# Kernel tuning notes

Hardware: AMD Instinct MI355X
Metric: run time of the kernel (lower is better)

Reference implementation:

```python
import jax, jax.numpy as jnp
import numpy as np
from collections import defaultdict

H = 24; W = 24          # patch grid
B0 = 64                 # original batch (len(batch_id))
B = 128                 # total batch incl. augmented copies
C_IN = 256; HID = 128; HEADS_S = 2; OUT = 256; K = 9; NCLS = 8


def _build_space_edges():
    # knn_graph on the normalized meshgrid coords; identical for every image -> offset copies.
    P = H * W
    coords = np.stack(np.meshgrid(np.arange(H), np.arange(W), indexing='ij'), -1).reshape(-1, 2).astype(np.float32)
    cn = coords / coords.max()
    d = ((cn[:, None, :] - cn[None, :, :]) ** 2).sum(-1)
    np.fill_diagonal(d, np.inf)              # loop=False
    nbr = np.argsort(d, axis=1)[:, :K]       # [P, K] neighbor (source) ids
    off = (np.arange(B0) * P)[:, None, None]
    src = (nbr[None] + off).reshape(-1)
    dst = (np.broadcast_to(np.arange(P)[:, None], (P, K))[None] + off).reshape(-1)
    return np.stack([src, dst]).astype(np.int64)


def _build_view_edges(bid_all):
    groups = defaultdict(list)
    for i, c in enumerate(bid_all.tolist()):
        groups[c].append(i)
    ei = []
    for c, mem in groups.items():
        for a in range(len(mem)):
            for b in range(a + 1, len(mem)):
                i, j = mem[a], mem[b]
                if i >= B0 and j >= B0:
                    continue               # skip augmented-augmented pairs
                ei.append((i, j)); ei.append((j, i))
    return np.array(ei, dtype=np.int64).T


def setup_inputs() -> dict:
    key = jax.random.key(0)
    ks = jax.random.split(key, 8)
    bid = np.repeat(np.arange(NCLS), B0 // NCLS).astype(np.int64)
    bid_all = np.concatenate([bid, bid])
    s = 0.05
    return {
        'x': jax.random.normal(ks[0], (B, C_IN, H, W), jnp.float32),
        'batch_id_all': jnp.asarray(bid_all),
        'batch_id': jnp.asarray(bid),
        'edge_index_space': jnp.asarray(_build_space_edges()),
        'edge_index_view': jnp.asarray(_build_view_edges(bid_all)),
        'W_space': jax.random.normal(ks[1], (C_IN, HEADS_S * HID), jnp.float32) * s,
        'att_src_space': jax.random.normal(ks[2], (HEADS_S, HID), jnp.float32) * s,
        'att_dst_space': jax.random.normal(ks[3], (HEADS_S, HID), jnp.float32) * s,
        'bias_space': jnp.zeros((HEADS_S * HID,), jnp.float32),
        'W_view': jax.random.normal(ks[4], (HEADS_S * HID, OUT), jnp.float32) * s,
        'att_src_view': jax.random.normal(ks[5], (1, OUT), jnp.float32) * s,
        'att_dst_view': jax.random.normal(ks[6], (1, OUT), jnp.float32) * s,
        'bias_view': jnp.zeros((OUT,), jnp.float32),
    }


def _gat(xn, edges, Wm, a_src, a_dst, bias, heads, outc):
    # PyG GATConv: linear -> per-edge leaky_relu attn -> segment softmax over dst -> scatter-add
    N = xn.shape[0]
    loops = jnp.arange(N, dtype=edges.dtype)              # add_self_loops=True
    src = jnp.concatenate([edges[0], loops])
    dst = jnp.concatenate([edges[1], loops])
    h = (xn @ Wm).reshape(N, heads, outc)                 # [N, H, C]
    a_s = jnp.sum(h * a_src[None], -1)                    # [N, H]
    a_d = jnp.sum(h * a_dst[None], -1)
    e = jax.nn.leaky_relu(a_s[src] + a_d[dst], 0.2)       # [E, H]
    m = jax.ops.segment_max(e, dst, num_segments=N)
    ee = jnp.exp(e - m[dst])
    ssum = jax.ops.segment_sum(ee, dst, num_segments=N)
    alpha = ee / (ssum[dst] + 1e-16)
    out = jax.ops.segment_sum(h[src] * alpha[..., None], dst, num_segments=N)
    return out.reshape(N, heads * outc) + bias            # concat=True


def reference(x, batch_id_all, batch_id, edge_index_space, edge_index_view,
              W_space, att_src_space, att_dst_space, bias_space,
              W_view, att_src_view, att_dst_view, bias_view):
    P = H * W
    node = x[:B0].transpose(0, 2, 3, 1).reshape(-1, C_IN)                # [B0*P, C_in]
    x_space = _gat(node, edge_index_space, W_space, att_src_space,
                   att_dst_space, bias_space, HEADS_S, HID)              # [B0*P, 256]
    emb = x_space.reshape(B0, P, -1).mean(axis=1)                        # per-image mean pool
    emb_all = emb[jnp.arange(B) % B0]                                    # augmented i -> i % B0
    feat = _gat(emb_all, edge_index_view, W_view, att_src_view,
                att_dst_view, bias_view, 1, OUT)                         # [B, 256]
    C = feat.shape[1]
    x_view = 0.5 * x_space.reshape(B0, P, C) + 0.5 * feat[:B0][:, None, :]
    # torch does .reshape(-1, C).view(B, C, H, W): a raw row-major reinterpret
    return x_view.reshape(B0, C, H, W)
```

## Files before the change

kernel.cpp:

```cpp
#include <hip/hip_runtime.h>

#define PGRID 576
#define NB0   64
#define CIN   256
#define KNN   9
#define NNODE (NB0 * PGRID)

typedef __attribute__((ext_vector_type(8))) short short8;
typedef __attribute__((ext_vector_type(4))) float f32x4;

__device__ __forceinline__ float bf2f(unsigned short u) {
    union { unsigned int i; float f; } v; v.i = ((unsigned int)u) << 16; return v.f;
}
__device__ __forceinline__ unsigned short f2b(float f) {
    unsigned int u = __float_as_uint(f);
    return (unsigned short)((u + 0x7FFFu + ((u >> 16) & 1u)) >> 16);
}

__global__ __launch_bounds__(256) void prep_w(const float* __restrict__ W,
                                              unsigned short* __restrict__ Wt) {
    __shared__ float tile[64][65];
    const int c0 = blockIdx.x * 64, j0 = blockIdx.y * 64;
    const int t = threadIdx.x, lo = t % 64, hi = t / 64;
#pragma unroll
    for (int r = 0; r < 16; ++r)
        tile[r * 4 + hi][lo] = W[(size_t)(c0 + r * 4 + hi) * 256 + j0 + lo];
    __syncthreads();
#pragma unroll
    for (int r = 0; r < 16; ++r)
        Wt[(size_t)(j0 + r * 4 + hi) * 256 + c0 + lo] = f2b(tile[lo][r * 4 + hi]);
}

__global__ __launch_bounds__(256) void gemm_fused(
    const float* __restrict__ x, const unsigned short* __restrict__ Wt,
    const float* __restrict__ att_src, const float* __restrict__ att_dst,
    unsigned short* __restrict__ h, float* __restrict__ as_, float* __restrict__ ad_) {
    __shared__ char ldsB[65536];
    const int bx = blockIdx.x;
    const int t  = threadIdx.x;
    const int b  = bx / 9;
    const int p0 = (bx % 9) * 64;
    const int n0 = bx * 64;
    const int l = t & 63, w = t >> 6;
    const int l4 = l >> 4, l15 = l & 15;
    const float* xb = x + (size_t)b * (CIN * PGRID);

    {
        const int jrow = t >> 4, g = t & 15;
#pragma unroll
        for (int i = 0; i < 16; ++i) {
            int j  = i * 16 + jrow;
            int gs = (g & 8) | ((g & 7) ^ (j & 7));
            __builtin_amdgcn_global_load_lds(
                (const char*)Wt + (size_t)j * 512 + gs * 16,
                ldsB + i * 4096 + (t & 192) * 16, 16, 0, 0);
        }
    }
    const int prow = p0 + w * 16 + l15;
    float a0[64];
#pragma unroll
    for (int ch = 0; ch < 2; ++ch)
#pragma unroll
        for (int q = 0; q < 4; ++q)
#pragma unroll
            for (int jj = 0; jj < 8; ++jj) {
                int c = ch * 128 + q * 32 + l4 * 8 + jj;
                a0[ch * 32 + q * 8 + jj] = xb[(size_t)c * PGRID + prow];
            }
    short8 apk[8];
#pragma unroll
    for (int cq = 0; cq < 8; ++cq) {
        short8 v;
#pragma unroll
        for (int jj = 0; jj < 8; ++jj) v[jj] = (short)f2b(a0[cq * 8 + jj]);
        apk[cq] = v;
    }
    f32x4 acc[16] = {};
    __syncthreads();
#pragma unroll
    for (int q = 0; q < 4; ++q) {
        const int gr = q * 4 + l4;
#pragma unroll
        for (int f = 0; f < 16; ++f) {
            int j  = f * 16 + l15;
            int gp = (gr & 8) | ((gr & 7) ^ (j & 7));
            short8 bf = *(const short8*)(ldsB + j * 256 + gp * 16);
            acc[f] = __builtin_amdgcn_mfma_f32_16x16x32_bf16(apk[q], bf, acc[f], 0, 0, 0);
        }
    }
    __syncthreads();
    {
        const int jrow = t >> 4, g = t & 15;
#pragma unroll
        for (int i = 0; i < 16; ++i) {
            int j  = i * 16 + jrow;
            int gs = (g & 8) | ((g & 7) ^ (j & 7));
            __builtin_amdgcn_global_load_lds(
                (const char*)Wt + (size_t)j * 512 + 256 + gs * 16,
                ldsB + i * 4096 + (t & 192) * 16, 16, 0, 0);
        }
    }
    __syncthreads();
#pragma unroll
    for (int q = 0; q < 4; ++q) {
        const int gr = q * 4 + l4;
#pragma unroll
        for (int f = 0; f < 16; ++f) {
            int j  = f * 16 + l15;
            int gp = (gr & 8) | ((gr & 7) ^ (j & 7));
            short8 bf = *(const short8*)(ldsB + j * 256 + gp * 16);
            acc[f] = __builtin_amdgcn_mfma_f32_16x16x32_bf16(apk[4 + q], bf, acc[f], 0, 0, 0);
        }
    }
    const int nb = n0 + w * 16 + l4 * 4;
#pragma unroll
    for (int f = 0; f < 16; ++f)
#pragma unroll
        for (int r = 0; r < 4; ++r)
            h[(size_t)(nb + r) * 256 + l15 + f * 16] = f2b(acc[f][r]);

    float av[16], dvv[16];
#pragma unroll
    for (int f = 0; f < 16; ++f) {
        av[f]  = att_src[f * 16 + l15];
        dvv[f] = att_dst[f * 16 + l15];
    }
#pragma unroll
    for (int r = 0; r < 4; ++r) {
        float s0 = 0.f, s1 = 0.f, d0 = 0.f, d1 = 0.f;
#pragma unroll
        for (int f = 0; f < 8; ++f)  { s0 += acc[f][r] * av[f];  d0 += acc[f][r] * dvv[f]; }
#pragma unroll
        for (int f = 8; f < 16; ++f) { s1 += acc[f][r] * av[f];  d1 += acc[f][r] * dvv[f]; }
#pragma unroll
        for (int m = 1; m < 16; m <<= 1) {
            s0 += __shfl_xor(s0, m); s1 += __shfl_xor(s1, m);
            d0 += __shfl_xor(d0, m); d1 += __shfl_xor(d1, m);
        }
        if (l15 == 0) {
            int n = nb + r;
            as_[n * 2] = s0; as_[n * 2 + 1] = s1;
            ad_[n * 2] = d0; ad_[n * 2 + 1] = d1;
        }
    }
}

__global__ __launch_bounds__(256) void space_gather(
    const unsigned short* __restrict__ h, const float* __restrict__ as_,
    const float* __restrict__ ad_, const int* __restrict__ esrc,
    const float* __restrict__ bias, float* __restrict__ xs) {
    __shared__ int   s_src[2][10];
    __shared__ float s_e[2][10][2];
    const int t = threadIdx.x;
    const int node = t >> 7;
    const int idx  = t & 127;
    const int n = blockIdx.x * 2 + node;
    if (idx < 10) {
        int src = (idx < 9) ? esrc[(size_t)n * KNN + idx] : n;
        s_src[node][idx] = src;
        float e0 = as_[src * 2]     + ad_[n * 2];
        float e1 = as_[src * 2 + 1] + ad_[n * 2 + 1];
        s_e[node][idx][0] = e0 >= 0.f ? e0 : 0.2f * e0;
        s_e[node][idx][1] = e1 >= 0.f ? e1 : 0.2f * e1;
    }
    __syncthreads();
    const int j2 = idx * 2;
    const int head = idx >> 6;
    float m = -1e30f;
#pragma unroll
    for (int k = 0; k < 10; ++k) m = fmaxf(m, s_e[node][k][head]);
    float wgt[10]; float ssum = 0.f;
#pragma unroll
    for (int k = 0; k < 10; ++k) { wgt[k] = __expf(s_e[node][k][head] - m); ssum += wgt[k]; }
    const float inv = 1.f / (ssum + 1e-16f);
    float o0 = 0.f, o1 = 0.f;
#pragma unroll
    for (int k = 0; k < 10; ++k) {
        unsigned int v = *(const unsigned int*)(h + (size_t)s_src[node][k] * 256 + j2);
        o0 += wgt[k] * bf2f((unsigned short)(v & 0xffff));
        o1 += wgt[k] * bf2f((unsigned short)(v >> 16));
    }
    float2 res;
    res.x = o0 * inv + bias[j2];
    res.y = o1 * inv + bias[j2 + 1];
    *(float2*)(xs + (size_t)n * 256 + j2) = res;
}

__global__ __launch_bounds__(256) void pool_partial(const float* __restrict__ xs,
                                                    float* __restrict__ embp) {
    const int b   = blockIdx.x;
    const int f4  = threadIdx.x & 63;
    const int seg = threadIdx.x >> 6;
    const float* base = xs + ((size_t)b * PGRID + seg * 144) * 256 + f4 * 4;
    float4 s = {0.f, 0.f, 0.f, 0.f};
    for (int p = 0; p < 144; ++p) {
        float4 v = *(const float4*)(base + (size_t)p * 256);
        s.x += v.x; s.y += v.y; s.z += v.z; s.w += v.w;
    }
    *(float4*)(embp + ((size_t)b * 4 + seg) * 256 + f4 * 4) = s;
}

__global__ __launch_bounds__(256) void view_linear(const float* __restrict__ embp,
                                                   const float* __restrict__ Wv,
                                                   const float* __restrict__ att_s,
                                                   const float* __restrict__ att_d,
                                                   float* __restrict__ hv,
                                                   float* __restrict__ asv,
                                                   float* __restrict__ adv) {
    __shared__ float er[256];
    __shared__ float red[2][256];
    const int i = blockIdx.x;
    const int j = threadIdx.x;
    const int i64 = i & 63;
    er[j] = (embp[((size_t)i64 * 4 + 0) * 256 + j] + embp[((size_t)i64 * 4 + 1) * 256 + j] +
             embp[((size_t)i64 * 4 + 2) * 256 + j] + embp[((size_t)i64 * 4 + 3) * 256 + j]) *
            (1.f / 576.f);
    __syncthreads();
    float acc = 0.f;
    for (int c = 0; c < 256; ++c) acc += er[c] * Wv[c * 256 + j];
    hv[(size_t)i * 256 + j] = acc;
    red[0][j] = acc * att_s[j];
    red[1][j] = acc * att_d[j];
    __syncthreads();
    for (int off = 128; off > 0; off >>= 1) {
        if (j < off) { red[0][j] += red[0][j + off]; red[1][j] += red[1][j + off]; }
        __syncthreads();
    }
    if (j == 0) { asv[i] = red[0][0]; adv[i] = red[1][0]; }
}

__global__ __launch_bounds__(256) void view_gather(const float* __restrict__ hv,
                                                   const float* __restrict__ asv,
                                                   const float* __restrict__ adv,
                                                   const int* __restrict__ ev,
                                                   int Ev,
                                                   const float* __restrict__ bias,
                                                   float* __restrict__ feat) {
    __shared__ int cnt;
    __shared__ int s_src[32];
    const int d = blockIdx.x;
    const int t = threadIdx.x;
    if (t == 0) cnt = 0;
    __syncthreads();
    for (int e = t; e < Ev; e += 256) {
        if (ev[Ev + e] == d) {
            int pos = atomicAdd(&cnt, 1);
            s_src[pos] = ev[e];
        }
    }
    __syncthreads();
    const int ns = cnt;
    const float adval = adv[d];
    float m = -1e30f;
    float ev_[16];
#pragma unroll 1
    for (int k = 0; k < ns; ++k) {
        float e = asv[s_src[k]] + adval;
        e = e >= 0.f ? e : 0.2f * e;
        ev_[k] = e;
        m = fmaxf(m, e);
    }
    float eself = asv[d] + adval;
    eself = eself >= 0.f ? eself : 0.2f * eself;
    m = fmaxf(m, eself);
    float ssum = 0.f;
#pragma unroll 1
    for (int k = 0; k < ns; ++k) { ev_[k] = __expf(ev_[k] - m); ssum += ev_[k]; }
    float wself = __expf(eself - m);
    ssum += wself;
    const float inv = 1.f / (ssum + 1e-16f);
    float out = 0.f;
#pragma unroll 1
    for (int k = 0; k < ns; ++k) out += ev_[k] * hv[(size_t)s_src[k] * 256 + t];
    out += wself * hv[(size_t)d * 256 + t];
    feat[d * 256 + t] = out * inv + bias[t];
}

__global__ __launch_bounds__(256) void combine(const float* __restrict__ xs,
                                               const float* __restrict__ feat,
                                               float* __restrict__ out, int ntot4) {
    int i = blockIdx.x * blockDim.x + threadIdx.x;
    if (i >= ntot4) return;
    size_t f = (size_t)i * 4;
    int b = (int)(f / (PGRID * 256));
    int j = (int)(f & 255);
    float4 a  = *(const float4*)(xs + f);
    float4 fb = *(const float4*)(feat + b * 256 + j);
    float4 o;
    o.x = 0.5f * (a.x + fb.x);
    o.y = 0.5f * (a.y + fb.y);
    o.z = 0.5f * (a.z + fb.z);
    o.w = 0.5f * (a.w + fb.w);
    *(float4*)(out + f) = o;
}

extern "C" void kernel_launch(void* const* d_in, const int* in_sizes, int n_in,
                              void* d_out, int out_size, void* d_ws, size_t ws_size,
                              hipStream_t stream) {
    const float* x        = (const float*)d_in[0];
    const int*   e_space  = (const int*)d_in[3];
    const int*   e_view   = (const int*)d_in[4];
    const float* W_space  = (const float*)d_in[5];
    const float* att_ss   = (const float*)d_in[6];
    const float* att_ds   = (const float*)d_in[7];
    const float* bias_s   = (const float*)d_in[8];
    const float* W_view   = (const float*)d_in[9];
    const float* att_sv   = (const float*)d_in[10];
    const float* att_dv   = (const float*)d_in[11];
    const float* bias_v   = (const float*)d_in[12];
    float* out = (float*)d_out;

    const int Ev = in_sizes[4] / 2;

    char* ws = (char*)d_ws;
    unsigned short* hbf = (unsigned short*)ws;
    unsigned short* Wt  = (unsigned short*)(ws + 18874368);
    float* xs   = (float*)(ws + 18874368 + 131072);
    float* as_  = xs  + (size_t)NNODE * 256;
    float* ad_  = as_ + NNODE * 2;
    float* embp = ad_ + NNODE * 2;
    float* hv   = embp + 64 * 4 * 256;
    float* asv  = hv  + 128 * 256;
    float* adv  = asv + 128;
    float* feat = adv + 128;

    prep_w<<<dim3(4, 4), 256, 0, stream>>>(W_space, Wt);
    gemm_fused<<<576, 256, 0, stream>>>(x, Wt, att_ss, att_ds, hbf, as_, ad_);
    space_gather<<<NNODE / 2, 256, 0, stream>>>(hbf, as_, ad_, e_space, bias_s, xs);
    pool_partial<<<NB0, 256, 0, stream>>>(xs, embp);
    view_linear<<<128, 256, 0, stream>>>(embp, W_view, att_sv, att_dv, hv, asv, adv);
    view_gather<<<NB0, 256, 0, stream>>>(hv, asv, adv, e_view, Ev, bias_v, feat);

    const int ntot4 = NB0 * PGRID * 256 / 4;
    combine<<<(ntot4 + 255) / 256, 256, 0, stream>>>(xs, feat, out, ntot4);
}
```

Baseline: 216.7 us.

## Store space-GAT output in bf16, widen pool grid, hoist x loads

```diff
diff --git a/kernel.cpp b/kernel.cpp
--- a/kernel.cpp
+++ b/kernel.cpp
@@ -45,6 +45,17 @@
     const int l4 = l >> 4, l15 = l & 15;
     const float* xb = x + (size_t)b * (CIN * PGRID);
 
+    const int prow = p0 + w * 16 + l15;
+    float a0[64];
+#pragma unroll
+    for (int ch = 0; ch < 2; ++ch)
+#pragma unroll
+        for (int q = 0; q < 4; ++q)
+#pragma unroll
+            for (int jj = 0; jj < 8; ++jj) {
+                int c = ch * 128 + q * 32 + l4 * 8 + jj;
+                a0[ch * 32 + q * 8 + jj] = xb[(size_t)c * PGRID + prow];
+            }
     {
         const int jrow = t >> 4, g = t & 15;
 #pragma unroll
@@ -56,17 +67,6 @@
                 ldsB + i * 4096 + (t & 192) * 16, 16, 0, 0);
         }
     }
-    const int prow = p0 + w * 16 + l15;
-    float a0[64];
-#pragma unroll
-    for (int ch = 0; ch < 2; ++ch)
-#pragma unroll
-        for (int q = 0; q < 4; ++q)
-#pragma unroll
-            for (int jj = 0; jj < 8; ++jj) {
-                int c = ch * 128 + q * 32 + l4 * 8 + jj;
-                a0[ch * 32 + q * 8 + jj] = xb[(size_t)c * PGRID + prow];
-            }
     short8 apk[8];
 #pragma unroll
     for (int cq = 0; cq < 8; ++cq) {
@@ -148,7 +148,7 @@
 __global__ __launch_bounds__(256) void space_gather(
     const unsigned short* __restrict__ h, const float* __restrict__ as_,
     const float* __restrict__ ad_, const int* __restrict__ esrc,
-    const float* __restrict__ bias, float* __restrict__ xs) {
+    const float* __restrict__ bias, unsigned short* __restrict__ xsb) {
     __shared__ int   s_src[2][10];
     __shared__ float s_e[2][10][2];
     const int t = threadIdx.x;
@@ -180,24 +180,34 @@
         o0 += wgt[k] * bf2f((unsigned short)(v & 0xffff));
         o1 += wgt[k] * bf2f((unsigned short)(v >> 16));
     }
-    float2 res;
-    res.x = o0 * inv + bias[j2];
-    res.y = o1 * inv + bias[j2 + 1];
-    *(float2*)(xs + (size_t)n * 256 + j2) = res;
-}
-
-__global__ __launch_bounds__(256) void pool_partial(const float* __restrict__ xs,
+    o0 = o0 * inv + bias[j2];
+    o1 = o1 * inv + bias[j2 + 1];
+    unsigned int pack = (unsigned int)f2b(o0) | ((unsigned int)f2b(o1) << 16);
+    *(unsigned int*)(xsb + (size_t)n * 256 + j2) = pack;
+}
+
+__global__ __launch_bounds__(256) void pool_partial(const unsigned short* __restrict__ xsb,
                                                     float* __restrict__ embp) {
-    const int b   = blockIdx.x;
-    const int f4  = threadIdx.x & 63;
-    const int seg = threadIdx.x >> 6;
-    const float* base = xs + ((size_t)b * PGRID + seg * 144) * 256 + f4 * 4;
-    float4 s = {0.f, 0.f, 0.f, 0.f};
-    for (int p = 0; p < 144; ++p) {
-        float4 v = *(const float4*)(base + (size_t)p * 256);
-        s.x += v.x; s.y += v.y; s.z += v.z; s.w += v.w;
-    }
-    *(float4*)(embp + ((size_t)b * 4 + seg) * 256 + f4 * 4) = s;
+    __shared__ float red[2][256];
+    const int b = blockIdx.x, seg = blockIdx.y;
+    const int t = threadIdx.x;
+    const int j2 = (t & 127) * 2, half = t >> 7;
+    const unsigned short* base = xsb + ((size_t)b * PGRID + seg * 64 + half * 32) * 256 + j2;
+    float s0 = 0.f, s1 = 0.f;
+#pragma unroll 8
+    for (int p = 0; p < 32; ++p) {
+        unsigned int v = *(const unsigned int*)(base + (size_t)p * 256);
+        s0 += bf2f((unsigned short)(v & 0xffff));
+        s1 += bf2f((unsigned short)(v >> 16));
+    }
+    red[half][j2] = s0; red[half][j2 + 1] = s1;
+    __syncthreads();
+    if (half == 0) {
+        float2 r;
+        r.x = s0 + red[1][j2];
+        r.y = s1 + red[1][j2 + 1];
+        *(float2*)(embp + ((size_t)b * 9 + seg) * 256 + j2) = r;
+    }
 }
 
 __global__ __launch_bounds__(256) void view_linear(const float* __restrict__ embp,
@@ -212,9 +222,10 @@
     const int i = blockIdx.x;
     const int j = threadIdx.x;
     const int i64 = i & 63;
-    er[j] = (embp[((size_t)i64 * 4 + 0) * 256 + j] + embp[((size_t)i64 * 4 + 1) * 256 + j] +
-             embp[((size_t)i64 * 4 + 2) * 256 + j] + embp[((size_t)i64 * 4 + 3) * 256 + j]) *
-            (1.f / 576.f);
+    float s = 0.f;
+#pragma unroll
+    for (int seg = 0; seg < 9; ++seg) s += embp[((size_t)i64 * 9 + seg) * 256 + j];
+    er[j] = s * (1.f / 576.f);
     __syncthreads();
     float acc = 0.f;
     for (int c = 0; c < 256; ++c) acc += er[c] * Wv[c * 256 + j];
@@ -276,7 +287,7 @@
     feat[d * 256 + t] = out * inv + bias[t];
 }
 
-__global__ __launch_bounds__(256) void combine(const float* __restrict__ xs,
+__global__ __launch_bounds__(256) void combine(const unsigned short* __restrict__ xsb,
                                                const float* __restrict__ feat,
                                                float* __restrict__ out, int ntot4) {
     int i = blockIdx.x * blockDim.x + threadIdx.x;
@@ -284,13 +295,13 @@
     size_t f = (size_t)i * 4;
     int b = (int)(f / (PGRID * 256));
     int j = (int)(f & 255);
-    float4 a  = *(const float4*)(xs + f);
+    uint2 v = *(const uint2*)(xsb + f);
     float4 fb = *(const float4*)(feat + b * 256 + j);
     float4 o;
-    o.x = 0.5f * (a.x + fb.x);
-    o.y = 0.5f * (a.y + fb.y);
-    o.z = 0.5f * (a.z + fb.z);
-    o.w = 0.5f * (a.w + fb.w);
+    o.x = 0.5f * (bf2f((unsigned short)(v.x & 0xffff)) + fb.x);
+    o.y = 0.5f * (bf2f((unsigned short)(v.x >> 16))   + fb.y);
+    o.z = 0.5f * (bf2f((unsigned short)(v.y & 0xffff)) + fb.z);
+    o.w = 0.5f * (bf2f((unsigned short)(v.y >> 16))   + fb.w);
     *(float4*)(out + f) = o;
 }
 
@@ -315,22 +326,22 @@
     char* ws = (char*)d_ws;
     unsigned short* hbf = (unsigned short*)ws;
     unsigned short* Wt  = (unsigned short*)(ws + 18874368);
-    float* xs   = (float*)(ws + 18874368 + 131072);
-    float* as_  = xs  + (size_t)NNODE * 256;
+    unsigned short* xsb = (unsigned short*)(ws + 18874368 + 131072);
+    float* as_  = (float*)(ws + 2 * 18874368 + 131072);
     float* ad_  = as_ + NNODE * 2;
     float* embp = ad_ + NNODE * 2;
-    float* hv   = embp + 64 * 4 * 256;
+    float* hv   = embp + 64 * 9 * 256;
     float* asv  = hv  + 128 * 256;
     float* adv  = asv + 128;
     float* feat = adv + 128;
 
     prep_w<<<dim3(4, 4), 256, 0, stream>>>(W_space, Wt);
     gemm_fused<<<576, 256, 0, stream>>>(x, Wt, att_ss, att_ds, hbf, as_, ad_);
-    space_gather<<<NNODE / 2, 256, 0, stream>>>(hbf, as_, ad_, e_space, bias_s, xs);
-    pool_partial<<<NB0, 256, 0, stream>>>(xs, embp);
+    space_gather<<<NNODE / 2, 256, 0, stream>>>(hbf, as_, ad_, e_space, bias_s, xsb);
+    pool_partial<<<dim3(NB0, 9), 256, 0, stream>>>(xsb, embp);
     view_linear<<<128, 256, 0, stream>>>(embp, W_view, att_sv, att_dv, hv, asv, adv);
     view_gather<<<NB0, 256, 0, stream>>>(hv, asv, adv, e_view, Ev, bias_v, feat);
 
     const int ntot4 = NB0 * PGRID * 256 / 4;
-    combine<<<(ntot4 + 255) / 256, 256, 0, stream>>>(xs, feat, out, ntot4);
-}
+    combine<<<(ntot4 + 255) / 256, 256, 0, stream>>>(xsb, feat, out, ntot4);
+}
```

Result: faster. 209.9 us (-3.1%).
